# Kernel optimization log

Measured on AMD Instinct MI355X. Metric: run time of the kernel, lower is better.

Reference implementation:

```python
import jax, jax.numpy as jnp
import numpy as np

B, L, D = 64, 256, 768
LABELS = 200
REL_OFF = 256  # to_pos[k] = k + 256


def setup_inputs() -> dict:
    key = jax.random.key(0)
    ks = jax.random.split(key, 8)
    return {
        "sequence_output": jax.random.normal(ks[0], (B, L, D), dtype=jnp.float32),
        "pos_embedding": jax.random.normal(ks[1], (2 * REL_OFF + 1, D), dtype=jnp.float32) * 0.02,
        "class_embedding": jax.random.normal(ks[2], (LABELS + 1, D), dtype=jnp.float32) * 0.02,
        "W": jax.random.normal(ks[3], (LABELS, 3 * D), dtype=jnp.float32) * 0.02,
        "b": jnp.zeros((LABELS,), dtype=jnp.float32),
        "head_indexes": jax.random.randint(ks[4], (B, L), 0, L),
        "frame": jax.random.randint(ks[5], (B,), 0, LABELS + 1),
        "pos": jax.random.randint(ks[6], (B,), 0, L),
    }


def reference(sequence_output, pos_embedding, class_embedding, W, b, head_indexes, frame, pos):
    # per-batch gather of token rows: sequence_output[i] = sequence_output[i][head_indexes[i]]
    gathered = jnp.take_along_axis(sequence_output, head_indexes[:, :, None], axis=1)  # [B,L,D]

    j = jnp.arange(sequence_output.shape[1])  # [L]
    rel = j[None, :] - pos[:, None] + REL_OFF  # [B,L] in [0, 512]
    pe = pos_embedding[rel]  # [B,L,D]

    # frame embedding only at j == pos[i], else class_embedding[0]
    fe_hit = class_embedding[frame]  # [B,D]
    is_pos = (j[None, :] == pos[:, None])[:, :, None]  # [B,L,1]
    fe = jnp.where(is_pos, fe_hit[:, None, :], class_embedding[0][None, None, :])  # [B,L,D]

    feat = jnp.concatenate([gathered, pe, fe], axis=-1)  # [B,L,3D]
    # dropout is identity at inference; classifier linear
    return jnp.einsum("blf,cf->blc", feat, W) + b
```

## Files before the change

### kernel.cpp

```cpp
#include <hip/hip_runtime.h>
#include <stdint.h>


typedef __attribute__((ext_vector_type(8))) short short8;
typedef __attribute__((ext_vector_type(4))) float f32x4;

#define AS1 __attribute__((address_space(1)))
#define AS3 __attribute__((address_space(3)))

#define TILE_STRIDE 12288
#define NT         13
#define NPE_RT     33
#define NCE_RT     13
#define NLOG_BLK   ((NPE_RT + NCE_RT) * NT)
#define NPACK_BLK  39
#define PEL_OFF_F  79872
#define CEL_OFF_F  189696
#define WS_NEED_B  931840

__device__ __forceinline__ unsigned short f2bf(float f) {
    union { float f; unsigned int u; } v; v.f = f;
    unsigned int u = v.u;
    return (unsigned short)((u + 0x7fffu + ((u >> 16) & 1u)) >> 16);
}

__device__ __forceinline__ short8 pack8(f32x4 a, f32x4 b) {
    short8 r;
    r[0] = (short)f2bf(a.x); r[1] = (short)f2bf(a.y);
    r[2] = (short)f2bf(a.z); r[3] = (short)f2bf(a.w);
    r[4] = (short)f2bf(b.x); r[5] = (short)f2bf(b.y);
    r[6] = (short)f2bf(b.z); r[7] = (short)f2bf(b.w);
    return r;
}

__device__ __forceinline__ void dma16(const unsigned short* g, AS3 unsigned short* l) {
    __builtin_amdgcn_global_load_lds((AS1 const unsigned int*)g,
                                     (AS3 unsigned int*)l, 16, 0, 0);
}

__global__ __launch_bounds__(512) void prep_kernel(
    const float* __restrict__ pe,
    const float* __restrict__ ce,
    const float* __restrict__ W,
    const float* __restrict__ bias,
    unsigned short* __restrict__ ws)
{
    __shared__ float red[8 * 256];

    if (blockIdx.x >= NLOG_BLK) {
        const int g   = (blockIdx.x - NLOG_BLK) * 512 + threadIdx.x;
        const int n   = g & 15;
        const int kb8 = (g >> 4) % 96;
        const int t   = g / 1536;
        const int row = t * 16 + n;
        const int col = kb8 * 8;
        f32x4 a = {0.f, 0.f, 0.f, 0.f}, b = {0.f, 0.f, 0.f, 0.f};
        if (row < 200) {
            const float* p = W + (size_t)row * 2304 + col;
            a = *(const f32x4*)p;
            b = *(const f32x4*)(p + 4);
        }
        *(short8*)(ws + (size_t)g * 8) = pack8(a, b);
        return;
    }

    const int bb   = blockIdx.x;
    const int w    = threadIdx.x >> 6;
    const int lane = threadIdx.x & 63;
    const int n16  = lane & 15;
    const int quad = lane >> 4;

    float* wsF = (float*)ws;
    int rowtile, t, nrows, koff;
    const float* A;
    float* outL;
    bool isCe;
    if (bb < NPE_RT * NT) {
        isCe = false; rowtile = bb / NT; t = bb % NT;
        nrows = 513; koff = 768;  A = pe; outL = wsF + PEL_OFF_F;
    } else {
        const int b2 = bb - NPE_RT * NT;
        isCe = true;  rowtile = b2 / NT; t = b2 % NT;
        nrows = 201; koff = 1536; A = ce; outL = wsF + CEL_OFF_F;
    }

    int arow = rowtile * 16 + n16;
    if (arow >= nrows) arow = nrows - 1;
    const float* abase = A + (size_t)arow * 768 + w * 96 + quad * 8;

    const int col  = t * 16 + n16;
    const int wrow = (col < 200) ? col : 0;
    const float* wbase = W + (size_t)wrow * 2304 + koff + w * 96 + quad * 8;

    f32x4 av0[3], av1[3], wv0[3], wv1[3];
#pragma unroll
    for (int ks = 0; ks < 3; ++ks) {
        av0[ks] = *(const f32x4*)(abase + ks * 32);
        av1[ks] = *(const f32x4*)(abase + ks * 32 + 4);
        wv0[ks] = *(const f32x4*)(wbase + ks * 32);
        wv1[ks] = *(const f32x4*)(wbase + ks * 32 + 4);
    }
    f32x4 acc = (f32x4){0.f, 0.f, 0.f, 0.f};
#pragma unroll
    for (int ks = 0; ks < 3; ++ks)
        acc = __builtin_amdgcn_mfma_f32_16x16x32_bf16(
            pack8(av0[ks], av1[ks]), pack8(wv0[ks], wv1[ks]), acc, 0, 0, 0);

#pragma unroll
    for (int r = 0; r < 4; ++r)
        red[w * 256 + lane * 4 + r] = acc[r];
    __syncthreads();
    if (threadIdx.x < 64) {
        const float bv = (isCe && col < 200) ? bias[col] : 0.0f;
#pragma unroll
        for (int r = 0; r < 4; ++r) {
            float s = 0.f;
#pragma unroll
            for (int ww = 0; ww < 8; ++ww)
                s += red[ww * 256 + lane * 4 + r];
            const int row = rowtile * 16 + quad * 4 + r;
            if (row < nrows)
                outL[(size_t)row * 208 + col] = s + bv;
        }
    }
}

__global__ __launch_bounds__(512, 4) void gemm_kernel(
    const unsigned short* __restrict__ ws,
    const float* __restrict__ seq,
    const int*   __restrict__ head,
    const int*   __restrict__ frame,
    const int*   __restrict__ pos,
    float* __restrict__ out)
{
    __shared__ unsigned short lds[4096 + 13 * 2048];

    const unsigned short* Wp = ws;
    const float* wsF = (const float*)ws;
    const float* peL = wsF + PEL_OFF_F;
    const float* ceL = wsF + CEL_OFF_F;

    const int tid  = threadIdx.x;
    const int wave = tid >> 6;
    const int lane = tid & 63;
    const int n16  = lane & 15;
    const int quad = lane >> 4;

    const int mblk    = blockIdx.x;
    const int i       = mblk >> 3;
    const int pos_i   = pos[i];
    const int frame_i = frame[i];

    const int sfm = wave & 1;
    const int sk  = wave >> 1;
    const int srow = mblk * 32 + sfm * 16 + n16;
    const int hi   = head[srow];
    const float* aP = seq + ((size_t)i * 256 + hi) * 768 + sk * 32 + quad * 8;
    unsigned short* aDst = (unsigned short*)lds + ((sfm * 4 + sk) * 64 + lane) * 8;

    const int p = wave & 1;
    const int q = wave >> 1;
    const unsigned short* aRd = lds + p * 2048 + lane * 8;
    const unsigned short* bRd[4];
    bool uok[4];
#pragma unroll
    for (int u = 0; u < 4; ++u) {
        const int t = q + 4 * u;
        uok[u] = (t < NT);
        bRd[u] = lds + 4096 + (uok[u] ? t : 0) * 2048 + quad * 128 + n16 * 8;
    }

    f32x4 acc[4];
#pragma unroll
    for (int u = 0; u < 4; ++u)
        acc[u] = (f32x4){0.f, 0.f, 0.f, 0.f};

    f32x4 a0 = *(const f32x4*)(aP);
    f32x4 a1 = *(const f32x4*)(aP + 4);

    for (int cc = 0; cc < 6; ++cc) {
        *(short8*)aDst = pack8(a0, a1);
#pragma unroll
        for (int un = wave; un < 52; un += 8) {
            const int t = un >> 2, part = un & 3;
            dma16(Wp + (size_t)t * TILE_STRIDE + cc * 2048 + part * 512 + lane * 8,
                  (AS3 unsigned short*)lds + 4096 + t * 2048 + part * 512 + lane * 8);
        }
        __syncthreads();
        if (cc < 5) {
            const float* ap = aP + (cc + 1) * 128;
            a0 = *(const f32x4*)(ap);
            a1 = *(const f32x4*)(ap + 4);
        }
#pragma unroll
        for (int ks = 0; ks < 4; ++ks) {
            short8 af = *(const short8*)(aRd + ks * 512);
#pragma unroll
            for (int u = 0; u < 4; ++u) {
                if (uok[u]) {
                    short8 bf = *(const short8*)(bRd[u] + ks * 512);
                    acc[u] = __builtin_amdgcn_mfma_f32_16x16x32_bf16(af, bf, acc[u], 0, 0, 0);
                }
            }
        }
        __syncthreads();
    }

    const int rbase = mblk * 32 + p * 16 + quad * 4;
#pragma unroll
    for (int u = 0; u < 4; ++u) {
        if (uok[u]) {
            const int col = (q + 4 * u) * 16 + n16;
            if (col < 200) {
#pragma unroll
                for (int r = 0; r < 4; ++r) {
                    const int row = rbase + r;
                    const int l   = row & 255;
                    const int rel = l - pos_i + 256;
                    const int cls = (l == pos_i) ? frame_i : 0;
                    out[(size_t)row * 200 + col] =
                        acc[u][r] + peL[(size_t)rel * 208 + col]
                                  + ceL[(size_t)cls * 208 + col];
                }
            }
        }
    }
}

__global__ __launch_bounds__(256) void gemm_fallback(
    const float* __restrict__ seq, const float* __restrict__ pe,
    const float* __restrict__ ce, const float* __restrict__ Wf,
    const float* __restrict__ bias, const int* __restrict__ head,
    const int* __restrict__ frame, const int* __restrict__ pos,
    float* __restrict__ out)
{
    const int tid  = threadIdx.x;
    const int wave = tid >> 6;
    const int lane = tid & 63;
    const int n16  = lane & 15;
    const int quad = lane >> 4;

    const int mrow  = blockIdx.x * 16 + n16;
    const int i     = mrow >> 8;
    const int j     = mrow & 255;
    const int pos_i = pos[i];
    const int hi    = head[mrow];
    const int rel   = j - pos_i + 256;
    const int cls   = (j == pos_i) ? frame[i] : 0;

    const float* segs[3];
    segs[0] = seq + ((size_t)i * 256 + (size_t)hi) * 768 + quad * 8;
    segs[1] = pe + (size_t)rel * 768 + quad * 8;
    segs[2] = ce + (size_t)cls * 768 + quad * 8;

    const int ntl = (wave == 0) ? 4 : 3;
    f32x4 acc[4];
#pragma unroll
    for (int u = 0; u < 4; ++u) {
        const int t = wave + 4 * u;
        const int col = t * 16 + n16;
        const float bv = (t < 13 && col < 200) ? bias[col] : 0.0f;
        acc[u] = (f32x4){bv, bv, bv, bv};
    }

    for (int s = 0; s < 3; ++s) {
        const float* ap = segs[s];
#pragma unroll 2
        for (int kk = 0; kk < 768; kk += 32) {
            short8 afr = pack8(*(const f32x4*)(ap + kk), *(const f32x4*)(ap + kk + 4));
#pragma unroll
            for (int u = 0; u < 4; ++u) {
                if (u < ntl) {
                    const int t = wave + 4 * u;
                    const int row = t * 16 + n16;
                    short8 bfr = {0, 0, 0, 0, 0, 0, 0, 0};
                    if (row < 200) {
                        const float* qp = Wf + (size_t)row * 2304 + s * 768 + kk + quad * 8;
                        bfr = pack8(*(const f32x4*)qp, *(const f32x4*)(qp + 4));
                    }
                    acc[u] = __builtin_amdgcn_mfma_f32_16x16x32_bf16(afr, bfr, acc[u], 0, 0, 0);
                }
            }
        }
    }

    const int rbase = blockIdx.x * 16 + quad * 4;
#pragma unroll
    for (int u = 0; u < 4; ++u) {
        const int t = wave + 4 * u;
        if (t < 13) {
            const int col = t * 16 + n16;
            if (col < 200) {
#pragma unroll
                for (int r = 0; r < 4; ++r)
                    out[(size_t)(rbase + r) * 200 + col] = acc[u][r];
            }
        }
    }
}

extern "C" void kernel_launch(void* const* d_in, const int* in_sizes, int n_in,
                              void* d_out, int out_size, void* d_ws, size_t ws_size,
                              hipStream_t stream) {
    const float* seq  = (const float*)d_in[0];
    const float* pe   = (const float*)d_in[1];
    const float* ce   = (const float*)d_in[2];
    const float* W    = (const float*)d_in[3];
    const float* bias = (const float*)d_in[4];
    const int* head   = (const int*)d_in[5];
    const int* frame  = (const int*)d_in[6];
    const int* pos    = (const int*)d_in[7];
    float* out = (float*)d_out;

    if (d_ws != nullptr && ws_size >= (size_t)WS_NEED_B) {
        unsigned short* ws = (unsigned short*)d_ws;
        prep_kernel<<<NLOG_BLK + NPACK_BLK, 512, 0, stream>>>(pe, ce, W, bias, ws);
        gemm_kernel<<<512, 512, 0, stream>>>(ws, seq, head, frame, pos, out);
    } else {
        gemm_fallback<<<1024, 256, 0, stream>>>(seq, pe, ce, W, bias, head,
                                                frame, pos, out);
    }
}
```

Before: 120.0 us.

## Fuse prep and GEMM kernels into one cooperative launch with grid sync

Merges the weight-packing/logit-table prep kernel and the main GEMM kernel into a single cooperative kernel. Each block first does its share of the prep work, then all blocks meet at a grid-wide barrier before running the GEMM body. This removes one kernel launch and the gap between the two kernels. In exchange it adds a grid sync, ties the prep work to a 512-block grid, and falls back to two launches if the cooperative launch fails.

```diff
diff --git a/kernel.cpp b/kernel.cpp
--- a/kernel.cpp
+++ b/kernel.cpp
@@ -1,5 +1,8 @@
 #include <hip/hip_runtime.h>
+#include <hip/hip_cooperative_groups.h>
 #include <stdint.h>
+
+namespace cg = cooperative_groups;
 
 
 typedef __attribute__((ext_vector_type(8))) short short8;
@@ -12,11 +15,12 @@
 #define NT         13
 #define NPE_RT     33
 #define NCE_RT     13
-#define NLOG_BLK   ((NPE_RT + NCE_RT) * NT)
-#define NPACK_BLK  39
+#define NLOG      ((NPE_RT + NCE_RT) * NT)
+#define NPACK      19968
 #define PEL_OFF_F  79872
 #define CEL_OFF_F  189696
 #define WS_NEED_B  931840
+#define GRID       512
 
 __device__ __forceinline__ unsigned short f2bf(float f) {
     union { float f; unsigned int u; } v; v.f = f;
@@ -38,39 +42,35 @@
                                      (AS3 unsigned int*)l, 16, 0, 0);
 }
 
-__global__ __launch_bounds__(512) void prep_kernel(
-    const float* __restrict__ pe,
-    const float* __restrict__ ce,
-    const float* __restrict__ W,
-    const float* __restrict__ bias,
-    unsigned short* __restrict__ ws)
-{
-    __shared__ float red[8 * 256];
-
-    if (blockIdx.x >= NLOG_BLK) {
-        const int g   = (blockIdx.x - NLOG_BLK) * 512 + threadIdx.x;
-        const int n   = g & 15;
-        const int kb8 = (g >> 4) % 96;
-        const int t   = g / 1536;
-        const int row = t * 16 + n;
-        const int col = kb8 * 8;
-        f32x4 a = {0.f, 0.f, 0.f, 0.f}, b = {0.f, 0.f, 0.f, 0.f};
-        if (row < 200) {
-            const float* p = W + (size_t)row * 2304 + col;
-            a = *(const f32x4*)p;
-            b = *(const f32x4*)(p + 4);
-        }
-        *(short8*)(ws + (size_t)g * 8) = pack8(a, b);
-        return;
-    }
-
-    const int bb   = blockIdx.x;
+__device__ __forceinline__ void pack_unit(int g, const float* __restrict__ W,
+                                          unsigned short* __restrict__ ws) {
+    const int n   = g & 15;
+    const int kb8 = (g >> 4) % 96;
+    const int t   = g / 1536;
+    const int row = t * 16 + n;
+    const int col = kb8 * 8;
+    f32x4 a = {0.f, 0.f, 0.f, 0.f}, b = {0.f, 0.f, 0.f, 0.f};
+    if (row < 200) {
+        const float* p = W + (size_t)row * 2304 + col;
+        a = *(const f32x4*)p;
+        b = *(const f32x4*)(p + 4);
+    }
+    *(short8*)(ws + (size_t)g * 8) = pack8(a, b);
+}
+
+__device__ void logits_tile(int bb,
+                            const float* __restrict__ pe,
+                            const float* __restrict__ ce,
+                            const float* __restrict__ W,
+                            const float* __restrict__ bias,
+                            float* __restrict__ wsF,
+                            float* red)
+{
     const int w    = threadIdx.x >> 6;
     const int lane = threadIdx.x & 63;
     const int n16  = lane & 15;
     const int quad = lane >> 4;
 
-    float* wsF = (float*)ws;
     int rowtile, t, nrows, koff;
     const float* A;
     float* outL;
@@ -106,6 +106,7 @@
         acc = __builtin_amdgcn_mfma_f32_16x16x32_bf16(
             pack8(av0[ks], av1[ks]), pack8(wv0[ks], wv1[ks]), acc, 0, 0, 0);
 
+    __syncthreads();
 #pragma unroll
     for (int r = 0; r < 4; ++r)
         red[w * 256 + lane * 4 + r] = acc[r];
@@ -125,16 +126,15 @@
     }
 }
 
-__global__ __launch_bounds__(512, 4) void gemm_kernel(
-    const unsigned short* __restrict__ ws,
-    const float* __restrict__ seq,
-    const int*   __restrict__ head,
-    const int*   __restrict__ frame,
-    const int*   __restrict__ pos,
-    float* __restrict__ out)
-{
-    __shared__ unsigned short lds[4096 + 13 * 2048];
-
+__device__ void gemm_body(unsigned short* lds,
+                          const unsigned short* __restrict__ ws,
+                          const float* __restrict__ seq,
+                          const int*   __restrict__ head,
+                          const int*   __restrict__ frame,
+                          const int*   __restrict__ pos,
+                          float* __restrict__ out,
+                          int mblk)
+{
     const unsigned short* Wp = ws;
     const float* wsF = (const float*)ws;
     const float* peL = wsF + PEL_OFF_F;
@@ -146,7 +146,6 @@
     const int n16  = lane & 15;
     const int quad = lane >> 4;
 
-    const int mblk    = blockIdx.x;
     const int i       = mblk >> 3;
     const int pos_i   = pos[i];
     const int frame_i = frame[i];
@@ -156,7 +155,7 @@
     const int srow = mblk * 32 + sfm * 16 + n16;
     const int hi   = head[srow];
     const float* aP = seq + ((size_t)i * 256 + hi) * 768 + sk * 32 + quad * 8;
-    unsigned short* aDst = (unsigned short*)lds + ((sfm * 4 + sk) * 64 + lane) * 8;
+    unsigned short* aDst = lds + ((sfm * 4 + sk) * 64 + lane) * 8;
 
     const int p = wave & 1;
     const int q = wave >> 1;
@@ -225,6 +224,64 @@
             }
         }
     }
+}
+
+__global__ __launch_bounds__(512, 4) void fused_kernel(
+    unsigned short* __restrict__ ws,
+    const float* __restrict__ seq,
+    const float* __restrict__ pe,
+    const float* __restrict__ ce,
+    const float* __restrict__ W,
+    const float* __restrict__ bias,
+    const int*   __restrict__ head,
+    const int*   __restrict__ frame,
+    const int*   __restrict__ pos,
+    float* __restrict__ out)
+{
+    __shared__ unsigned short lds[4096 + 13 * 2048];
+
+    {
+        const int g = blockIdx.x * 512 + threadIdx.x;
+        if (g < NPACK)
+            pack_unit(g, W, ws);
+        float* red = (float*)lds;
+        logits_tile(blockIdx.x, pe, ce, W, bias, (float*)ws, red);
+        if (blockIdx.x + GRID < NLOG)
+            logits_tile(blockIdx.x + GRID, pe, ce, W, bias, (float*)ws, red);
+    }
+    __threadfence();
+    cg::this_grid().sync();
+
+    gemm_body(lds, ws, seq, head, frame, pos, out, blockIdx.x);
+}
+
+__global__ __launch_bounds__(512) void prep_kernel(
+    const float* __restrict__ pe,
+    const float* __restrict__ ce,
+    const float* __restrict__ W,
+    const float* __restrict__ bias,
+    unsigned short* __restrict__ ws)
+{
+    __shared__ float red[2048];
+    if (blockIdx.x < NLOG) {
+        logits_tile(blockIdx.x, pe, ce, W, bias, (float*)ws, red);
+    } else {
+        const int g = (blockIdx.x - NLOG) * 512 + threadIdx.x;
+        if (g < NPACK)
+            pack_unit(g, W, ws);
+    }
+}
+
+__global__ __launch_bounds__(512, 4) void gemm_kernel(
+    const unsigned short* __restrict__ ws,
+    const float* __restrict__ seq,
+    const int*   __restrict__ head,
+    const int*   __restrict__ frame,
+    const int*   __restrict__ pos,
+    float* __restrict__ out)
+{
+    __shared__ unsigned short lds[4096 + 13 * 2048];
+    gemm_body(lds, ws, seq, head, frame, pos, out, blockIdx.x);
 }
 
 __global__ __launch_bounds__(256) void gemm_fallback(
@@ -314,8 +371,17 @@
 
     if (d_ws != nullptr && ws_size >= (size_t)WS_NEED_B) {
         unsigned short* ws = (unsigned short*)d_ws;
-        prep_kernel<<<NLOG_BLK + NPACK_BLK, 512, 0, stream>>>(pe, ce, W, bias, ws);
-        gemm_kernel<<<512, 512, 0, stream>>>(ws, seq, head, frame, pos, out);
+        void* kargs[] = {(void*)&ws, (void*)&seq, (void*)&pe, (void*)&ce,
+                         (void*)&W, (void*)&bias, (void*)&head, (void*)&frame,
+                         (void*)&pos, (void*)&out};
+        hipError_t e = hipLaunchCooperativeKernel((const void*)fused_kernel,
+                                                  dim3(GRID), dim3(512),
+                                                  kargs, 0, stream);
+        if (e != hipSuccess) {
+            prep_kernel<<<NLOG + (NPACK + 511) / 512, 512, 0, stream>>>(
+                pe, ce, W, bias, ws);
+            gemm_kernel<<<GRID, 512, 0, stream>>>(ws, seq, head, frame, pos, out);
+        }
     } else {
         gemm_fallback<<<1024, 256, 0, stream>>>(seq, pe, ce, W, bias, head,
                                                 frame, pos, out);
```

Result: slower. 291.6 us (+143.0%).

## Double-buffer GEMM K-chunks in LDS and swizzle block order

Applied to the files above, without the earlier changes.

The GEMM K loop moves from six 128-wide chunks with two barriers each to twelve 64-wide chunks held in two LDS buffers. The DMA for the next chunk and the A-row loads are issued before computing on the current buffer, and there is one barrier per chunk. Only waves 4-7 now stage the gathered A rows. The block index is also remapped so that neighbouring blocks take different batches. This aims to overlap global-to-LDS transfer with MFMA work and cut barrier stalls, but it changes LDS layout and indexing in ways that need careful checking.

```diff
diff --git a/kernel.cpp b/kernel.cpp
--- a/kernel.cpp
+++ b/kernel.cpp
@@ -12,8 +12,8 @@
 #define NT         13
 #define NPE_RT     33
 #define NCE_RT     13
-#define NLOG_BLK   ((NPE_RT + NCE_RT) * NT)
-#define NPACK_BLK  39
+#define NLOG      ((NPE_RT + NCE_RT) * NT)
+#define NPACK      19968
 #define PEL_OFF_F  79872
 #define CEL_OFF_F  189696
 #define WS_NEED_B  931840
@@ -45,10 +45,10 @@
     const float* __restrict__ bias,
     unsigned short* __restrict__ ws)
 {
-    __shared__ float red[8 * 256];
-
-    if (blockIdx.x >= NLOG_BLK) {
-        const int g   = (blockIdx.x - NLOG_BLK) * 512 + threadIdx.x;
+    __shared__ float red[2048];
+
+    if (blockIdx.x >= NLOG) {
+        const int g   = (blockIdx.x - NLOG) * 512 + threadIdx.x;
         const int n   = g & 15;
         const int kb8 = (g >> 4) % 96;
         const int t   = g / 1536;
@@ -133,7 +133,7 @@
     const int*   __restrict__ pos,
     float* __restrict__ out)
 {
-    __shared__ unsigned short lds[4096 + 13 * 2048];
+    __shared__ unsigned short lds[30720];
 
     const unsigned short* Wp = ws;
     const float* wsF = (const float*)ws;
@@ -146,28 +146,38 @@
     const int n16  = lane & 15;
     const int quad = lane >> 4;
 
-    const int mblk    = blockIdx.x;
+    const int mblk = ((blockIdx.x & 7) << 6) | (blockIdx.x >> 3);
+
     const int i       = mblk >> 3;
     const int pos_i   = pos[i];
     const int frame_i = frame[i];
 
+    const bool aStg = (wave >= 4);
     const int sfm = wave & 1;
-    const int sk  = wave >> 1;
-    const int srow = mblk * 32 + sfm * 16 + n16;
-    const int hi   = head[srow];
-    const float* aP = seq + ((size_t)i * 256 + hi) * 768 + sk * 32 + quad * 8;
-    unsigned short* aDst = (unsigned short*)lds + ((sfm * 4 + sk) * 64 + lane) * 8;
+    const int sks = (wave >> 1) & 1;
+    const float* aP = nullptr;
+    if (aStg) {
+        const int srow = mblk * 32 + sfm * 16 + n16;
+        const int hi   = head[srow];
+        aP = seq + ((size_t)i * 256 + hi) * 768 + quad * 8;
+    }
+    unsigned short* aW0 = lds + (sfm * 2 + sks) * 512 + lane * 8;
+    unsigned short* aW1 = aW0 + 2048;
 
     const int p = wave & 1;
     const int q = wave >> 1;
-    const unsigned short* aRd = lds + p * 2048 + lane * 8;
-    const unsigned short* bRd[4];
+    const unsigned short* aR0 = lds + p * 1024 + lane * 8;
+    const unsigned short* aR1 = aR0 + 2048;
+    const unsigned short* bR0[4];
+    const unsigned short* bR1[4];
     bool uok[4];
 #pragma unroll
     for (int u = 0; u < 4; ++u) {
         const int t = q + 4 * u;
         uok[u] = (t < NT);
-        bRd[u] = lds + 4096 + (uok[u] ? t : 0) * 2048 + quad * 128 + n16 * 8;
+        const int off = (uok[u] ? t : 0) * 1024 + quad * 128 + n16 * 8;
+        bR0[u] = lds + 4096 + off;
+        bR1[u] = lds + 17408 + off;
     }
 
     f32x4 acc[4];
@@ -175,36 +185,72 @@
     for (int u = 0; u < 4; ++u)
         acc[u] = (f32x4){0.f, 0.f, 0.f, 0.f};
 
-    f32x4 a0 = *(const f32x4*)(aP);
-    f32x4 a1 = *(const f32x4*)(aP + 4);
-
-    for (int cc = 0; cc < 6; ++cc) {
-        *(short8*)aDst = pack8(a0, a1);
-#pragma unroll
-        for (int un = wave; un < 52; un += 8) {
-            const int t = un >> 2, part = un & 3;
-            dma16(Wp + (size_t)t * TILE_STRIDE + cc * 2048 + part * 512 + lane * 8,
-                  (AS3 unsigned short*)lds + 4096 + t * 2048 + part * 512 + lane * 8);
-        }
+    f32x4 a0 = {0,0,0,0}, a1 = {0,0,0,0};
+
+    if (aStg) {
+        a0 = *(const f32x4*)(aP + sks * 32);
+        a1 = *(const f32x4*)(aP + sks * 32 + 4);
+    }
+#pragma unroll
+    for (int un = wave; un < 26; un += 8) {
+        const int t = un >> 1, hf = un & 1;
+        dma16(Wp + (size_t)t * TILE_STRIDE + hf * 512 + lane * 8,
+              (AS3 unsigned short*)lds + 4096 + t * 1024 + hf * 512 + lane * 8);
+    }
+    if (aStg) *(short8*)aW0 = pack8(a0, a1);
+    __syncthreads();
+
+#define COMPUTE(AR, BR)                                                        \
+    {                                                                          \
+        _Pragma("unroll")                                                      \
+        for (int ks = 0; ks < 2; ++ks) {                                       \
+            short8 af = *(const short8*)((AR) + ks * 512);                     \
+            _Pragma("unroll")                                                  \
+            for (int u = 0; u < 4; ++u) {                                      \
+                if (uok[u]) {                                                  \
+                    short8 bf = *(const short8*)((BR)[u] + ks * 512);          \
+                    acc[u] = __builtin_amdgcn_mfma_f32_16x16x32_bf16(          \
+                        af, bf, acc[u], 0, 0, 0);                              \
+                }                                                              \
+            }                                                                  \
+        }                                                                      \
+    }
+
+    for (int cp = 0; cp < 6; ++cp) {
+        const int c0 = 2 * cp, c1 = c0 + 1;
+        if (aStg) {
+            a0 = *(const f32x4*)(aP + c1 * 64 + sks * 32);
+            a1 = *(const f32x4*)(aP + c1 * 64 + sks * 32 + 4);
+        }
+#pragma unroll
+        for (int un = wave; un < 26; un += 8) {
+            const int t = un >> 1, hf = un & 1;
+            dma16(Wp + (size_t)t * TILE_STRIDE + c1 * 1024 + hf * 512 + lane * 8,
+                  (AS3 unsigned short*)lds + 17408 + t * 1024 + hf * 512 + lane * 8);
+        }
+        COMPUTE(aR0, bR0);
+        if (aStg) *(short8*)aW1 = pack8(a0, a1);
         __syncthreads();
-        if (cc < 5) {
-            const float* ap = aP + (cc + 1) * 128;
-            a0 = *(const f32x4*)(ap);
-            a1 = *(const f32x4*)(ap + 4);
-        }
-#pragma unroll
-        for (int ks = 0; ks < 4; ++ks) {
-            short8 af = *(const short8*)(aRd + ks * 512);
-#pragma unroll
-            for (int u = 0; u < 4; ++u) {
-                if (uok[u]) {
-                    short8 bf = *(const short8*)(bRd[u] + ks * 512);
-                    acc[u] = __builtin_amdgcn_mfma_f32_16x16x32_bf16(af, bf, acc[u], 0, 0, 0);
-                }
-            }
-        }
-        __syncthreads();
-    }
+
+        if (cp < 5) {
+            if (aStg) {
+                a0 = *(const f32x4*)(aP + (c0 + 2) * 64 + sks * 32);
+                a1 = *(const f32x4*)(aP + (c0 + 2) * 64 + sks * 32 + 4);
+            }
+#pragma unroll
+            for (int un = wave; un < 26; un += 8) {
+                const int t = un >> 1, hf = un & 1;
+                dma16(Wp + (size_t)t * TILE_STRIDE + (c0 + 2) * 1024 + hf * 512 + lane * 8,
+                      (AS3 unsigned short*)lds + 4096 + t * 1024 + hf * 512 + lane * 8);
+            }
+            COMPUTE(aR1, bR1);
+            if (aStg) *(short8*)aW0 = pack8(a0, a1);
+            __syncthreads();
+        } else {
+            COMPUTE(aR1, bR1);
+        }
+    }
+#undef COMPUTE
 
     const int rbase = mblk * 32 + p * 16 + quad * 4;
 #pragma unroll
@@ -314,7 +360,8 @@
 
     if (d_ws != nullptr && ws_size >= (size_t)WS_NEED_B) {
         unsigned short* ws = (unsigned short*)d_ws;
-        prep_kernel<<<NLOG_BLK + NPACK_BLK, 512, 0, stream>>>(pe, ce, W, bias, ws);
+        prep_kernel<<<NLOG + (NPACK + 511) / 512, 512, 0, stream>>>(
+            pe, ce, W, bias, ws);
         gemm_kernel<<<512, 512, 0, stream>>>(ws, seq, head, frame, pos, out);
     } else {
         gemm_fallback<<<1024, 256, 0, stream>>>(seq, pe, ce, W, bias, head,
```

New measurement: 125.0 us. 4.2% more time.
